# Kernel tuning notes

Measured on AMD Instinct MI355X. Metric: run time of the kernel, lower is better.

## Reference

```python
import jax, jax.numpy as jnp
import numpy as np

N_LAYERS = 24  # number of recurrent applications of the shared HashLinear


def setup_inputs() -> dict:
    key = jax.random.key(0)
    ks = jax.random.split(key, 9)
    B, D_IN, N, N_OUT = 1024, 784, 4096, 10
    s_in = 1.0 / np.sqrt(D_IN)
    s_h = 1.0 / np.sqrt(N)
    x = jax.random.normal(ks[0], (B, D_IN), jnp.float32)
    # nn.Linear(prod(input_dim), 2*n_units)
    W_in = jax.random.uniform(ks[1], (2 * N, D_IN), jnp.float32, -s_in, s_in)
    b_in = jax.random.uniform(ks[2], (2 * N,), jnp.float32, -s_in, s_in)
    # HashLinear(n_units, n_units, period=1, 'hash'): learnable +/-1 context key + shared linear
    key_sp = jnp.where(jax.random.bernoulli(ks[3], 0.5, (1, N)), 1.0, -1.0).astype(jnp.float32)
    W_sp = jax.random.uniform(ks[4], (N, N), jnp.float32, -s_h, s_h)
    b_sp = jax.random.uniform(ks[5], (N,), jnp.float32, -s_h, s_h)
    # HashLinear(n_units, 10, period=1, 'hash')
    key_f = jnp.where(jax.random.bernoulli(ks[6], 0.5, (1, N)), 1.0, -1.0).astype(jnp.float32)
    W_f = jax.random.uniform(ks[7], (N_OUT, N), jnp.float32, -s_h, s_h)
    b_f = jax.random.uniform(ks[8], (N_OUT,), jnp.float32, -s_h, s_h)
    return {"x": x, "W_in": W_in, "b_in": b_in, "key_sp": key_sp, "W_sp": W_sp,
            "b_sp": b_sp, "key_f": key_f, "W_f": W_f, "b_f": b_f, "time": 0}


def _hash_linear(xa, xb, o, W, b):
    # Superposition HashLinear: same shared weight applied to both streams,
    # each modulated by the +/-1 context key o ([n_in]).
    ya = (xa * o) @ W.T + b
    yb = (xb * o) @ W.T + b
    return ya, yb


def reference(x, W_in, b_in, key_sp, W_sp, b_sp, key_f, W_f, b_f, time):
    N = W_sp.shape[0]
    r = x @ W_in.T + b_in                 # [B, 2N]
    r_a, r_b = r[:, :N], r[:, N:]         # torch.split(r, n_units, 1)
    pre0 = r_a
    r_a, r_b = jax.nn.relu(r_a), jax.nn.relu(r_b)
    o = key_sp[time % key_sp.shape[0]]    # period=1, time=0 in the module

    def step(carry, _):
        a, b2 = carry
        ya, yb = _hash_linear(a, b2, o, W_sp, b_sp)
        return (jax.nn.relu(ya), jax.nn.relu(yb)), ya  # collect preactivation r_a

    (r_a, r_b), pres = jax.lax.scan(step, (r_a, r_b), None, length=N_LAYERS)
    of = key_f[time % key_f.shape[0]]
    out_a, out_b = _hash_linear(r_a, r_b, of, W_f, b_f)  # [B,10], [B,10]
    preactivations = jnp.concatenate([pre0[None], pres], axis=0)  # [N_LAYERS+1, B, N]
    return (out_a, out_b, preactivations)
```

## Files before the change

### kernel.cpp

```cpp
#include <hip/hip_runtime.h>
#include <hip/hip_bf16.h>
#include <stdint.h>

typedef __bf16 bf16x8 __attribute__((ext_vector_type(8)));
typedef float  f32x4  __attribute__((ext_vector_type(4)));

#define NH      4096
#define MB      1024
#define M2      2048
#define DIN     784
#define KPAD    832
#define N_IN    8192
#define NLAYERS 24
#define NOUT    10

#define ABUF    8192
#define BBUF    4096
#define BUFSTR  (2*ABUF + 2*BBUF)

__device__ __forceinline__ unsigned short f2bf(float x) {
  union { float f; unsigned u; } v; v.f = x;
  unsigned r = v.u + 0x7FFFu + ((v.u >> 16) & 1u);
  return (unsigned short)(r >> 16);
}
__device__ __forceinline__ float bf2f(unsigned short u) {
  union { unsigned u; float f; } v; v.u = ((unsigned)u) << 16; return v.f;
}

__device__ __forceinline__ void async16(const void* g, void* l) {
  __builtin_amdgcn_global_load_lds(
      (const __attribute__((address_space(1))) void*)g,
      (__attribute__((address_space(3))) void*)l, 16, 0, 0);
}

__global__ void k_conv_wsp(const float* __restrict__ W, const float* __restrict__ o,
                           unsigned short* __restrict__ out) {
  size_t i = ((size_t)blockIdx.x * blockDim.x + threadIdx.x) * 4;
  if (i >= (size_t)NH * NH) return;
  float4 w = *reinterpret_cast<const float4*>(W + i);
  int k = (int)(i & (NH - 1));
  float4 ov = *reinterpret_cast<const float4*>(o + k);
  ushort4 r;
  r.x = f2bf(w.x * ov.x); r.y = f2bf(w.y * ov.y);
  r.z = f2bf(w.z * ov.z); r.w = f2bf(w.w * ov.w);
  *reinterpret_cast<ushort4*>(out + i) = r;
}

__global__ void k_conv_pad(const float* __restrict__ in, unsigned short* __restrict__ out,
                           int rows, int kin, int kout) {
  size_t i = (size_t)blockIdx.x * blockDim.x + threadIdx.x;
  if (i >= (size_t)rows * kout) return;
  int r = (int)(i / kout), c = (int)(i % kout);
  out[i] = (c < kin) ? f2bf(in[(size_t)r * kin + c]) : (unsigned short)0;
}

__device__ __forceinline__ void gemm_core(
    const unsigned short* __restrict__ Ag, const unsigned short* __restrict__ Bg,
    int K, int bm, int bn, unsigned short* lds, f32x4 acc[4][4])
{
  const int t    = threadIdx.x;
  const int lane = t & 63;
  const int wave = t >> 6;
  const int wm   = wave >> 1;
  const int wn   = wave & 1;
  const int l15  = lane & 15;
  const int lk8  = (lane >> 4) * 8;

  unsigned aOffG[2]; int aOffL[2];
#pragma unroll
  for (int j = 0; j < 2; ++j) {
    const int d   = (j * 512 + t) * 16;
    const int row = d >> 6;
    const int l   = d ^ (((row >> 1) & 3) << 4);
    aOffL[j] = d >> 1;
    aOffG[j] = (unsigned)((bm + row) * K + ((l & 63) >> 1));
  }
  unsigned bOffG; int bOffL;
  {
    const int d   = t * 16;
    const int row = d >> 6;
    const int l   = d ^ (((row >> 1) & 3) << 4);
    bOffL = d >> 1;
    bOffG = (unsigned)((bn + row) * K + ((l & 63) >> 1));
  }

  int aRd[4], bRd[4];
#pragma unroll
  for (int i = 0; i < 4; ++i) {
    const int ra = wm * 64 + i * 16 + l15;
    aRd[i] = ((ra * 64 + lk8 * 2) ^ (((ra >> 1) & 3) << 4)) >> 1;
    const int rb = wn * 64 + i * 16 + l15;
    bRd[i] = ((rb * 64 + lk8 * 2) ^ (((rb >> 1) & 3) << 4)) >> 1;
  }

  auto STAGE = [&](int bufE, int k0, int kh) {
    const int khA = bufE + kh * ABUF;
    const int khB = bufE + 2 * ABUF + kh * BBUF;
    const unsigned kadd = (unsigned)(k0 + kh * 32);
    async16(Ag + aOffG[0] + kadd, lds + khA + aOffL[0]);
    async16(Ag + aOffG[1] + kadd, lds + khA + aOffL[1]);
    async16(Bg + bOffG    + kadd, lds + khB + bOffL);
  };

  auto SUBPHASE = [&](int cur, int kk, int nxt, int k0n, bool st, bool last) {
    if (last) asm volatile("s_waitcnt vmcnt(0)" ::: "memory");
    else      asm volatile("s_waitcnt vmcnt(3)" ::: "memory");
    __builtin_amdgcn_s_barrier();
    __builtin_amdgcn_sched_barrier(0);
    if (st) STAGE(nxt, k0n, kk);
    const int kkA = cur + kk * ABUF;
    const int kkB = cur + 2 * ABUF + kk * BBUF;
    bf16x8 af[4], bv[4];
#pragma unroll
    for (int i = 0; i < 4; ++i) af[i] = *reinterpret_cast<const bf16x8*>(lds + kkA + aRd[i]);
#pragma unroll
    for (int i = 0; i < 4; ++i) bv[i] = *reinterpret_cast<const bf16x8*>(lds + kkB + bRd[i]);
    asm volatile("s_waitcnt lgkmcnt(0)" ::: "memory");
    __builtin_amdgcn_sched_barrier(0);
    __builtin_amdgcn_s_setprio(1);
#pragma unroll
    for (int mi = 0; mi < 4; ++mi)
#pragma unroll
      for (int ni = 0; ni < 4; ++ni)
        acc[mi][ni] = __builtin_amdgcn_mfma_f32_16x16x32_bf16(af[mi], bv[ni], acc[mi][ni], 0, 0, 0);
    __builtin_amdgcn_s_setprio(0);
    __builtin_amdgcn_sched_barrier(0);
  };

  STAGE(0, 0, 0);
  STAGE(0, 0, 1);
  const int nt = K >> 6;
  for (int kt = 0; kt < nt; ++kt) {
    const int cur = (kt & 1) ? BUFSTR : 0;
    const int nxt = cur ^ BUFSTR;
    const bool st = (kt + 1 < nt);
    SUBPHASE(cur, 0, nxt, (kt + 1) << 6, st, false);
    SUBPHASE(cur, 1, nxt, (kt + 1) << 6, st, !st);
  }
}

__global__ __launch_bounds__(512, 2) void k_gemm_layer(
    const unsigned short* __restrict__ A, const unsigned short* __restrict__ W,
    const float* __restrict__ bias, float* __restrict__ preact,
    unsigned short* __restrict__ Anext)
{
  __shared__ __align__(16) unsigned short lds[2 * BUFSTR];
  const int bid = blockIdx.x;
  const int s   = ((bid & 7) << 5) + (bid >> 3);
  const int bm = (s >> 5) * 256;
  const int bn = (s & 31) * 128;
  f32x4 acc[4][4] = {};
  gemm_core(A, W, NH, bm, bn, lds, acc);

  const int lane = threadIdx.x & 63;
  const int wave = threadIdx.x >> 6;
  const int wm = (wave >> 1) * 64, wn = (wave & 1) * 64;
  const int l15 = lane & 15;
#pragma unroll
  for (int mi = 0; mi < 4; ++mi) {
    const int gm0 = bm + wm + mi * 16 + (lane >> 4) * 4;
#pragma unroll
    for (int ni = 0; ni < 4; ++ni) {
      const int gn = bn + wn + ni * 16 + l15;
      const float bv = bias[gn];
#pragma unroll
      for (int r = 0; r < 4; ++r) {
        const int gm = gm0 + r;
        const float y = acc[mi][ni][r] + bv;
        if (gm < MB) preact[(size_t)gm * NH + gn] = y;
        Anext[(size_t)gm * NH + gn] = f2bf(y > 0.f ? y : 0.f);
      }
    }
  }
}

__global__ __launch_bounds__(512, 2) void k_gemm_in(
    const unsigned short* __restrict__ X, const unsigned short* __restrict__ W,
    const float* __restrict__ bias, float* __restrict__ preact0,
    unsigned short* __restrict__ A0)
{
  __shared__ __align__(16) unsigned short lds[2 * BUFSTR];
  const int bid = blockIdx.x;
  const int s   = ((bid & 7) << 5) + (bid >> 3);
  const int bm = (s >> 6) * 256;
  const int bn = (s & 63) * 128;
  f32x4 acc[4][4] = {};
  gemm_core(X, W, KPAD, bm, bn, lds, acc);

  const int lane = threadIdx.x & 63;
  const int wave = threadIdx.x >> 6;
  const int wm = (wave >> 1) * 64, wn = (wave & 1) * 64;
  const int l15 = lane & 15;
#pragma unroll
  for (int mi = 0; mi < 4; ++mi) {
    const int gm0 = bm + wm + mi * 16 + (lane >> 4) * 4;
#pragma unroll
    for (int ni = 0; ni < 4; ++ni) {
      const int gn = bn + wn + ni * 16 + l15;
      const float bv = bias[gn];
#pragma unroll
      for (int r = 0; r < 4; ++r) {
        const int gm = gm0 + r;
        const float y = acc[mi][ni][r] + bv;
        const unsigned short rl = f2bf(y > 0.f ? y : 0.f);
        if (gn < NH) {
          preact0[(size_t)gm * NH + gn] = y;
          A0[(size_t)gm * NH + gn] = rl;
        } else {
          A0[(size_t)(MB + gm) * NH + (gn - NH)] = rl;
        }
      }
    }
  }
}

__global__ void k_final(const unsigned short* __restrict__ A,
                        const float* __restrict__ Wf, const float* __restrict__ of,
                        const float* __restrict__ bf_, float* __restrict__ out)
{
  const int m = blockIdx.x;
  const int t = threadIdx.x;
  float accj[NOUT] = {};
  for (int k = t; k < NH; k += 256) {
    const float a = bf2f(A[(size_t)m * NH + k]) * of[k];
#pragma unroll
    for (int j = 0; j < NOUT; ++j) accj[j] += a * Wf[j * NH + k];
  }
  __shared__ float red[4][NOUT];
#pragma unroll
  for (int j = 0; j < NOUT; ++j) {
    float v = accj[j];
    for (int off = 32; off > 0; off >>= 1) v += __shfl_down(v, off);
    if ((t & 63) == 0) red[t >> 6][j] = v;
  }
  __syncthreads();
  if (t < NOUT) {
    const float s = red[0][t] + red[1][t] + red[2][t] + red[3][t] + bf_[t];
    out[(size_t)m * NOUT + t] = s;
  }
}

extern "C" void kernel_launch(void* const* d_in, const int* in_sizes, int n_in,
                              void* d_out, int out_size, void* d_ws, size_t ws_size,
                              hipStream_t stream) {
  const float* x     = (const float*)d_in[0];
  const float* W_in  = (const float*)d_in[1];
  const float* b_in  = (const float*)d_in[2];
  const float* keysp = (const float*)d_in[3];
  const float* W_sp  = (const float*)d_in[4];
  const float* b_sp  = (const float*)d_in[5];
  const float* keyf  = (const float*)d_in[6];
  const float* W_f   = (const float*)d_in[7];
  const float* b_f   = (const float*)d_in[8];

  float* out    = (float*)d_out;
  float* preact = out + (size_t)2 * MB * NOUT;

  char* ws = (char*)d_ws;
  unsigned short* Wsp_bf = (unsigned short*)ws;  ws += (size_t)NH * NH * 2;
  unsigned short* A0     = (unsigned short*)ws;  ws += (size_t)M2 * NH * 2;
  unsigned short* A1     = (unsigned short*)ws;  ws += (size_t)M2 * NH * 2;
  unsigned short* Win_bf = (unsigned short*)ws;  ws += (size_t)N_IN * KPAD * 2;
  unsigned short* X_bf   = (unsigned short*)ws;  ws += (size_t)MB * KPAD * 2;

  k_conv_wsp<<<(NH * (size_t)NH / 4 + 255) / 256, 256, 0, stream>>>(W_sp, keysp, Wsp_bf);
  k_conv_pad<<<((size_t)N_IN * KPAD + 255) / 256, 256, 0, stream>>>(W_in, Win_bf, N_IN, DIN, KPAD);
  k_conv_pad<<<((size_t)MB * KPAD + 255) / 256, 256, 0, stream>>>(x, X_bf, MB, DIN, KPAD);

  k_gemm_in<<<256, 512, 0, stream>>>(X_bf, Win_bf, b_in, preact, A0);

  unsigned short* Ain = A0;
  unsigned short* Aout = A1;
  for (int tlay = 0; tlay < NLAYERS; ++tlay) {
    float* pre = preact + (size_t)(tlay + 1) * MB * NH;
    k_gemm_layer<<<256, 512, 0, stream>>>(Ain, Wsp_bf, b_sp, pre, Aout);
    unsigned short* tmp = Ain; Ain = Aout; Aout = tmp;
  }

  k_final<<<M2, 256, 0, stream>>>(Ain, W_f, keyf, b_f, out);
}
```

Baseline: 1.794 ms.

## Switch GEMM mainloop to triple-buffered full-K-tile pipeline with new LDS swizzle

The GEMM core moves from a double buffer split into two 32-wide K half-phases, each with its own barrier, to a three-slot LDS ring of full 64-wide K tiles. Loads are issued two tiles ahead and each tile waits on a single barrier. The LDS layout becomes 128-byte rows with an XOR-by-row swizzle to avoid bank conflicts on the fragment reads. This aims to hide global-to-LDS latency better and halve barrier count, at the cost of more LDS per block (about 144 KB) and more in-flight loads per thread.

Measured after the change: 1.758 ms. 2.0% less time.

```diff
diff --git a/kernel.cpp b/kernel.cpp
--- a/kernel.cpp
+++ b/kernel.cpp
@@ -14,9 +14,9 @@
 #define NLAYERS 24
 #define NOUT    10
 
-#define ABUF    8192
-#define BBUF    4096
-#define BUFSTR  (2*ABUF + 2*BBUF)
+#define ASLOT   (256 * 64)
+#define BSLOT   (128 * 64)
+#define SLOT    (ASLOT + BSLOT)
 
 __device__ __forceinline__ unsigned short f2bf(float x) {
   union { float f; unsigned u; } v; v.f = x;
@@ -64,78 +64,77 @@
   const int wm   = wave >> 1;
   const int wn   = wave & 1;
   const int l15  = lane & 15;
-  const int lk8  = (lane >> 4) * 8;
-
-  unsigned aOffG[2]; int aOffL[2];
+  const int lkb  = (lane >> 4) * 16;
+
+  unsigned aG[4]; int aL[4];
+#pragma unroll
+  for (int j = 0; j < 4; ++j) {
+    const int c   = j * 512 + t;
+    const int row = c >> 3;
+    const int sb  = ((c & 7) * 16) ^ ((row & 7) << 4);
+    aL[j] = c * 8;
+    aG[j] = (unsigned)((bm + row) * K + (sb >> 1));
+  }
+  unsigned bG[2]; int bL[2];
 #pragma unroll
   for (int j = 0; j < 2; ++j) {
-    const int d   = (j * 512 + t) * 16;
-    const int row = d >> 6;
-    const int l   = d ^ (((row >> 1) & 3) << 4);
-    aOffL[j] = d >> 1;
-    aOffG[j] = (unsigned)((bm + row) * K + ((l & 63) >> 1));
-  }
-  unsigned bOffG; int bOffL;
-  {
-    const int d   = t * 16;
-    const int row = d >> 6;
-    const int l   = d ^ (((row >> 1) & 3) << 4);
-    bOffL = d >> 1;
-    bOffG = (unsigned)((bn + row) * K + ((l & 63) >> 1));
-  }
-
-  int aRd[4], bRd[4];
-#pragma unroll
-  for (int i = 0; i < 4; ++i) {
-    const int ra = wm * 64 + i * 16 + l15;
-    aRd[i] = ((ra * 64 + lk8 * 2) ^ (((ra >> 1) & 3) << 4)) >> 1;
-    const int rb = wn * 64 + i * 16 + l15;
-    bRd[i] = ((rb * 64 + lk8 * 2) ^ (((rb >> 1) & 3) << 4)) >> 1;
-  }
-
-  auto STAGE = [&](int bufE, int k0, int kh) {
-    const int khA = bufE + kh * ABUF;
-    const int khB = bufE + 2 * ABUF + kh * BBUF;
-    const unsigned kadd = (unsigned)(k0 + kh * 32);
-    async16(Ag + aOffG[0] + kadd, lds + khA + aOffL[0]);
-    async16(Ag + aOffG[1] + kadd, lds + khA + aOffL[1]);
-    async16(Bg + bOffG    + kadd, lds + khB + bOffL);
+    const int c   = j * 512 + t;
+    const int row = c >> 3;
+    const int sb  = ((c & 7) * 16) ^ ((row & 7) << 4);
+    bL[j] = c * 8;
+    bG[j] = (unsigned)((bn + row) * K + (sb >> 1));
+  }
+
+  int aRd[2][4], bRd[2][4];
+#pragma unroll
+  for (int kk = 0; kk < 2; ++kk)
+#pragma unroll
+    for (int i = 0; i < 4; ++i) {
+      const int ra = wm * 64 + i * 16 + l15;
+      aRd[kk][i] = (ra * 128 + ((kk * 64 + lkb) ^ ((ra & 7) << 4))) >> 1;
+      const int rb = wn * 64 + i * 16 + l15;
+      bRd[kk][i] = (rb * 128 + ((kk * 64 + lkb) ^ ((rb & 7) << 4))) >> 1;
+    }
+
+  auto STAGE = [&](int slotIdx, int k0) {
+    unsigned short* s = lds + slotIdx * SLOT;
+#pragma unroll
+    for (int j = 0; j < 4; ++j) async16(Ag + aG[j] + (unsigned)k0, s + aL[j]);
+#pragma unroll
+    for (int j = 0; j < 2; ++j) async16(Bg + bG[j] + (unsigned)k0, s + ASLOT + bL[j]);
   };
 
-  auto SUBPHASE = [&](int cur, int kk, int nxt, int k0n, bool st, bool last) {
-    if (last) asm volatile("s_waitcnt vmcnt(0)" ::: "memory");
-    else      asm volatile("s_waitcnt vmcnt(3)" ::: "memory");
+  const int nt = K >> 6;
+  STAGE(0, 0);
+  if (nt > 1) STAGE(1, 64);
+
+  int s0 = 0;
+  int s2 = 2;
+  for (int kt = 0; kt < nt; ++kt) {
+    __builtin_amdgcn_sched_barrier(0);
+    if (kt + 1 < nt) asm volatile("s_waitcnt vmcnt(6)" ::: "memory");
+    else             asm volatile("s_waitcnt vmcnt(0)" ::: "memory");
     __builtin_amdgcn_s_barrier();
     __builtin_amdgcn_sched_barrier(0);
-    if (st) STAGE(nxt, k0n, kk);
-    const int kkA = cur + kk * ABUF;
-    const int kkB = cur + 2 * ABUF + kk * BBUF;
-    bf16x8 af[4], bv[4];
-#pragma unroll
-    for (int i = 0; i < 4; ++i) af[i] = *reinterpret_cast<const bf16x8*>(lds + kkA + aRd[i]);
-#pragma unroll
-    for (int i = 0; i < 4; ++i) bv[i] = *reinterpret_cast<const bf16x8*>(lds + kkB + bRd[i]);
-    asm volatile("s_waitcnt lgkmcnt(0)" ::: "memory");
-    __builtin_amdgcn_sched_barrier(0);
     __builtin_amdgcn_s_setprio(1);
-#pragma unroll
-    for (int mi = 0; mi < 4; ++mi)
-#pragma unroll
-      for (int ni = 0; ni < 4; ++ni)
-        acc[mi][ni] = __builtin_amdgcn_mfma_f32_16x16x32_bf16(af[mi], bv[ni], acc[mi][ni], 0, 0, 0);
+    if (kt + 2 < nt) STAGE(s2, (kt + 2) << 6);
+    const unsigned short* base = lds + s0 * SLOT;
+#pragma unroll
+    for (int kk = 0; kk < 2; ++kk) {
+      bf16x8 af[4], bv[4];
+#pragma unroll
+      for (int i = 0; i < 4; ++i) af[i] = *reinterpret_cast<const bf16x8*>(base + aRd[kk][i]);
+#pragma unroll
+      for (int i = 0; i < 4; ++i) bv[i] = *reinterpret_cast<const bf16x8*>(base + ASLOT + bRd[kk][i]);
+#pragma unroll
+      for (int mi = 0; mi < 4; ++mi)
+#pragma unroll
+        for (int ni = 0; ni < 4; ++ni)
+          acc[mi][ni] = __builtin_amdgcn_mfma_f32_16x16x32_bf16(af[mi], bv[ni], acc[mi][ni], 0, 0, 0);
+    }
     __builtin_amdgcn_s_setprio(0);
-    __builtin_amdgcn_sched_barrier(0);
-  };
-
-  STAGE(0, 0, 0);
-  STAGE(0, 0, 1);
-  const int nt = K >> 6;
-  for (int kt = 0; kt < nt; ++kt) {
-    const int cur = (kt & 1) ? BUFSTR : 0;
-    const int nxt = cur ^ BUFSTR;
-    const bool st = (kt + 1 < nt);
-    SUBPHASE(cur, 0, nxt, (kt + 1) << 6, st, false);
-    SUBPHASE(cur, 1, nxt, (kt + 1) << 6, st, !st);
+    s0 = (s0 == 2) ? 0 : s0 + 1;
+    s2 = (s2 == 2) ? 0 : s2 + 1;
   }
 }
 
@@ -144,7 +143,7 @@
     const float* __restrict__ bias, float* __restrict__ preact,
     unsigned short* __restrict__ Anext)
 {
-  __shared__ __align__(16) unsigned short lds[2 * BUFSTR];
+  __shared__ __align__(16) unsigned short lds[3 * SLOT];
   const int bid = blockIdx.x;
   const int s   = ((bid & 7) << 5) + (bid >> 3);
   const int bm = (s >> 5) * 256;
@@ -179,7 +178,7 @@
     const float* __restrict__ bias, float* __restrict__ preact0,
     unsigned short* __restrict__ A0)
 {
-  __shared__ __align__(16) unsigned short lds[2 * BUFSTR];
+  __shared__ __align__(16) unsigned short lds[3 * SLOT];
   const int bid = blockIdx.x;
   const int s   = ((bid & 7) << 5) + (bid >> 3);
   const int bm = (s >> 6) * 256;
```
